# Kernel tuning notes

Measured on AMD Instinct MI355X. Metric: run time of the kernel, lower is better.

Reference implementation:

```python
import jax, jax.numpy as jnp
import numpy as np

B, T, NH, HD, VD = 2, 2048, 16, 128, 256
KD = NH * HD            # 2048
VDIM = NH * VD          # 4096
EPS = 1e-12


def _l2norm(x):
    # torch.nn.functional.normalize: x / max(||x||_2, eps)
    n = jnp.sqrt(jnp.sum(x * x, axis=-1, keepdims=True))
    return x / jnp.maximum(n, EPS)


def setup_inputs() -> dict:
    key = jax.random.key(0)
    k1, k2 = jax.random.split(key)
    x = jax.random.normal(k1, (B, T, KD), dtype=jnp.float32)
    W = jax.random.normal(k2, (2 * KD + VDIM + 2 * NH, KD), dtype=jnp.float32) * 0.02
    state = jnp.zeros((B, NH, VD, HD), dtype=jnp.float32)
    return {"x": x, "W": W, "state": state}


def reference(x, W, state):
    # shared projection (no bias)
    proj = jnp.einsum('btd,od->bto', x, W)  # [B,T,2*KD+VDIM+2*NH]
    q = proj[..., :KD].reshape(B, T, NH, HD)
    k = proj[..., KD:2 * KD].reshape(B, T, NH, HD)
    v = proj[..., 2 * KD:2 * KD + VDIM].reshape(B, T, NH, VD)
    g = jax.nn.sigmoid(proj[..., 2 * KD + VDIM:2 * KD + VDIM + NH])      # [B,T,NH] decay gate
    beta = jax.nn.sigmoid(proj[..., 2 * KD + VDIM + NH:])                # [B,T,NH]
    q = _l2norm(q)
    k = _l2norm(k)

    # time-major for scan
    qs = jnp.moveaxis(q, 1, 0)      # [T,B,NH,HD]
    ks = jnp.moveaxis(k, 1, 0)
    vs = jnp.moveaxis(v, 1, 0)      # [T,B,NH,VD]
    gs = jnp.moveaxis(g, 1, 0)      # [T,B,NH]
    bs = jnp.moveaxis(beta, 1, 0)

    def step(S, inp):
        # gated delta rule: S_t = g*S - g*b*(S k) k^T + b*v k^T ; o_t = S_t q
        q_t, k_t, v_t, g_t, b_t = inp
        Sk = jnp.einsum('bnvh,bnh->bnv', S, k_t)                         # [B,NH,VD]
        delta = b_t[..., None] * (v_t - g_t[..., None] * Sk)             # [B,NH,VD]
        S_new = g_t[..., None, None] * S + delta[..., None] * k_t[:, :, None, :]
        o = jnp.einsum('bnvh,bnh->bnv', S_new, q_t)                      # [B,NH,VD]
        return S_new, o

    _, out = jax.lax.scan(step, state, (qs, ks, vs, gs, bs))
    return jnp.moveaxis(out, 0, 1)  # [B,T,NH,VD]
```

## Files before the change

kernel.cpp:

```cpp
#include <hip/hip_runtime.h>
#include <hip/hip_bf16.h>
#include <cstdint>


typedef __attribute__((ext_vector_type(8))) short short8;
typedef __attribute__((ext_vector_type(4))) float f32x4;
typedef unsigned short u16;

using as1_void = __attribute__((address_space(1))) void;
using as3_void = __attribute__((address_space(3))) void;

__device__ __forceinline__ void gll16(const void* g, void* l) {
  __builtin_amdgcn_global_load_lds((const as1_void*)g, (as3_void*)l, 16, 0, 0);
}

__device__ __forceinline__ u16 bf16_rne(float f) {
  union { float f; uint32_t u; } x; x.f = f;
  uint32_t u = x.u;
  return (u16)((u + 0x7fffu + ((u >> 16) & 1u)) >> 16);
}
__device__ __forceinline__ float bf2f(u16 v) {
  union { uint32_t u; float f; } x; x.u = (uint32_t)v << 16;
  return x.f;
}

#define LGKM_BAR() do {                                      \
    asm volatile("s_waitcnt lgkmcnt(0)" ::: "memory");       \
    __builtin_amdgcn_s_barrier();                            \
    __builtin_amdgcn_sched_barrier(0);                       \
  } while (0)

#define SCHED_FENCE() __builtin_amdgcn_sched_barrier(0)
#define HW_BAR() __builtin_amdgcn_s_barrier()
#define LGKM0() asm volatile("s_waitcnt lgkmcnt(0)" ::: "memory")
#define VMCNT(n) asm volatile("s_waitcnt vmcnt(" #n ")" ::: "memory")

__global__ __launch_bounds__(256) void cvt_f32_bf16(const float* __restrict__ in,
                                                    u16* __restrict__ out, int n4) {
  int i = blockIdx.x * 256 + threadIdx.x;
  if (i < n4) {
    float4 v = ((const float4*)in)[i];
    ushort4 o;
    o.x = bf16_rne(v.x); o.y = bf16_rne(v.y);
    o.z = bf16_rne(v.z); o.w = bf16_rne(v.w);
    ((ushort4*)out)[i] = o;
  }
}

__global__ __launch_bounds__(256, 1) void gate_kernel(const float* __restrict__ x,
                                                      const float* __restrict__ W,
                                                      float* __restrict__ gbuf,
                                                      u16* __restrict__ xb) {
  const int w = threadIdx.x >> 6, lane = threadIdx.x & 63;
  const int r0 = (blockIdx.x * 4 + w) * 4;
  const float* xr = x + (size_t)r0 * 2048 + lane * 32;
  float4 xv[4][8];
#pragma unroll
  for (int i = 0; i < 4; ++i)
#pragma unroll
    for (int j = 0; j < 8; ++j)
      xv[i][j] = ((const float4*)(xr + (size_t)i * 2048))[j];
#pragma unroll
  for (int i = 0; i < 4; ++i) {
    u16* xrow = xb + (size_t)(r0 + i) * 2048 + lane * 32;
#pragma unroll
    for (int j = 0; j < 8; ++j) {
      ushort4 o;
      o.x = bf16_rne(xv[i][j].x); o.y = bf16_rne(xv[i][j].y);
      o.z = bf16_rne(xv[i][j].z); o.w = bf16_rne(xv[i][j].w);
      ((ushort4*)xrow)[j] = o;
    }
  }
  for (int col = 0; col < 32; ++col) {
    const float* wp = W + (size_t)(8192 + col) * 2048 + lane * 32;
    float4 wv[8];
#pragma unroll
    for (int j = 0; j < 8; ++j) wv[j] = ((const float4*)wp)[j];
    float d[4] = {0.f, 0.f, 0.f, 0.f};
#pragma unroll
    for (int i = 0; i < 4; ++i)
#pragma unroll
      for (int j = 0; j < 8; ++j)
        d[i] += xv[i][j].x * wv[j].x + xv[i][j].y * wv[j].y +
                xv[i][j].z * wv[j].z + xv[i][j].w * wv[j].w;
#pragma unroll
    for (int i = 0; i < 4; ++i) {
      d[i] += __shfl_xor(d[i], 1);  d[i] += __shfl_xor(d[i], 2);
      d[i] += __shfl_xor(d[i], 4);  d[i] += __shfl_xor(d[i], 8);
      d[i] += __shfl_xor(d[i], 16); d[i] += __shfl_xor(d[i], 32);
    }
    if (lane == 0) {
#pragma unroll
      for (int i = 0; i < 4; ++i) {
        int rv = r0 + i, b = rv >> 11, t = rv & 2047;
        float s = 1.f / (1.f + __expf(-d[i]));
        gbuf[((size_t)(b * 16 + (col & 15)) * 2048 + t) * 2 + (col >> 4)] = s;
      }
    }
  }
}

__global__ __launch_bounds__(512, 2) void gemm_bf16_btn(const u16* __restrict__ A,
                                                        const u16* __restrict__ B,
                                                        u16* __restrict__ qb,
                                                        u16* __restrict__ kb,
                                                        u16* __restrict__ vb) {
  __shared__ __align__(16) u16 As[2][16384];
  __shared__ __align__(16) u16 Bs[2][16384];
  __shared__ float nrm[2][4][128];

  const int tid = threadIdx.x;
  const int wid = tid >> 6, lane = tid & 63;
  const int lr = lane & 15, lk = lane >> 4;
  const int wr = wid >> 2, wc = wid & 3;

  const int wg = ((blockIdx.x & 7) << 6) | (blockIdx.x >> 3);
  const int bm = wg >> 5, bn = wg & 31;

  const int e8s = (tid & 7) ^ (((tid >> 3) & 1) << 2) ^ (((tid >> 5) & 1) << 1);
  const int srow = tid >> 3;
  const u16* Agb = A + (size_t)(bm * 256 + srow) * 2048 + e8s * 8;
  const u16* Bgb = B + (size_t)(bn * 256 + srow) * 2048 + e8s * 8;

  const int kkx = lr & 1;
  const int lkp = lk ^ (((lr >> 2) & 1) << 1);
  const int aOff0 = (wr * 128 + lr) * 64 + kkx * 32 + lkp * 8;
  const int aOff1 = (wr * 128 + lr) * 64 + (1 ^ kkx) * 32 + lkp * 8;
  const int bOff0 = (wc * 64 + lr) * 64 + kkx * 32 + lkp * 8;
  const int bOff1 = (wc * 64 + lr) * 64 + (1 ^ kkx) * 32 + lkp * 8;

  auto stageA = [&](int bf, int kt, int h) {
    const u16* s = Agb + (size_t)(h * 128) * 2048 + kt * 64;
    u16* d = &As[bf][h * 8192 + wid * 512];
    gll16(s, d);
    gll16(s + (size_t)64 * 2048, d + 4096);
  };
  auto stageB = [&](int bf, int kt, int h) {
    const u16* s = Bgb + (size_t)(h * 128) * 2048 + kt * 64;
    u16* d = &Bs[bf][h * 8192 + wid * 512];
    gll16(s, d);
    gll16(s + (size_t)64 * 2048, d + 4096);
  };

  f32x4 acc[8][4] = {};

  stageA(0, 0, 0); stageA(0, 0, 1);
  stageB(0, 0, 0); stageB(0, 0, 1);
  stageA(1, 1, 0); stageA(1, 1, 1);
  stageB(1, 1, 0);
  VMCNT(6);
  SCHED_FENCE();
  HW_BAR();

#define QUAD(M0, N0)                                                          \
  do {                                                                        \
    __builtin_amdgcn_s_setprio(1);                                            \
    _Pragma("unroll")                                                         \
    for (int m_ = 0; m_ < 4; ++m_)                                            \
      _Pragma("unroll")                                                       \
      for (int n_ = 0; n_ < 2; ++n_) {                                        \
        acc[M0 + m_][N0 + n_] = __builtin_amdgcn_mfma_f32_16x16x32_bf16(      \
            a[M0 + m_][0], b[N0 + n_][0], acc[M0 + m_][N0 + n_], 0, 0, 0);    \
        acc[M0 + m_][N0 + n_] = __builtin_amdgcn_mfma_f32_16x16x32_bf16(      \
            a[M0 + m_][1], b[N0 + n_][1], acc[M0 + m_][N0 + n_], 0, 0, 0);    \
      }                                                                       \
    __builtin_amdgcn_s_setprio(0);                                            \
  } while (0)

  for (int kt = 0; kt < 32; ++kt) {
    const int bf = kt & 1;
    const u16* pA0 = &As[bf][aOff0];
    const u16* pA1 = &As[bf][aOff1];
    const u16* pB0 = &Bs[bf][bOff0];
    const u16* pB1 = &Bs[bf][bOff1];
    short8 a[8][2], b[4][2];

#pragma unroll
    for (int m = 0; m < 8; ++m) {
      a[m][0] = *(const short8*)(pA0 + m * 1024);
      a[m][1] = *(const short8*)(pA1 + m * 1024);
    }
#pragma unroll
    for (int n = 0; n < 2; ++n) {
      b[n][0] = *(const short8*)(pB0 + n * 1024);
      b[n][1] = *(const short8*)(pB1 + n * 1024);
    }
    SCHED_FENCE();
    if (kt < 31) stageB((kt + 1) & 1, kt + 1, 1);
    SCHED_FENCE(); HW_BAR(); LGKM0(); SCHED_FENCE();
    QUAD(0, 0);
    SCHED_FENCE(); HW_BAR();

#pragma unroll
    for (int n = 2; n < 4; ++n) {
      b[n][0] = *(const short8*)(pB0 + n * 1024);
      b[n][1] = *(const short8*)(pB1 + n * 1024);
    }
    SCHED_FENCE();
    if (kt < 30) stageA(bf, kt + 2, 0);
    SCHED_FENCE(); HW_BAR(); LGKM0(); SCHED_FENCE();
    QUAD(0, 2);
    SCHED_FENCE(); HW_BAR();

    if (kt < 30) stageA(bf, kt + 2, 1);
    SCHED_FENCE(); HW_BAR(); SCHED_FENCE();
    QUAD(4, 0);
    SCHED_FENCE(); HW_BAR();

    if (kt < 30) stageB(bf, kt + 2, 0);
    SCHED_FENCE(); HW_BAR(); SCHED_FENCE();
    QUAD(4, 2);
    SCHED_FENCE();
    if (kt < 30) { VMCNT(6); } else if (kt == 30) { VMCNT(0); }
    SCHED_FENCE(); HW_BAR();
  }
#undef QUAD

  if (bn < 16) {
#pragma unroll
    for (int m = 0; m < 8; ++m)
#pragma unroll
      for (int r = 0; r < 4; ++r) {
        float s = 0.f;
#pragma unroll
        for (int nn = 0; nn < 4; ++nn) {
          float v = bf2f(bf16_rne(acc[m][nn][r]));
          s += v * v;
        }
        s += __shfl_xor(s, 1); s += __shfl_xor(s, 2);
        s += __shfl_xor(s, 4); s += __shfl_xor(s, 8);
        if (lr == 0) nrm[wr][wc][m * 16 + lk * 4 + r] = s;
      }
    __syncthreads();
#pragma unroll
    for (int m = 0; m < 8; ++m)
#pragma unroll
      for (int r = 0; r < 4; ++r) {
        int rloc = m * 16 + lk * 4 + r;
        float ss = nrm[wr][wc][rloc] + nrm[wr][wc ^ 1][rloc];
        float sc = 1.f / fmaxf(sqrtf(ss), 1e-12f);
        int row = bm * 256 + wr * 128 + rloc;
        int bb = row >> 11, tt = row & 2047;
#pragma unroll
        for (int nn = 0; nn < 4; ++nn) {
          int col = bn * 256 + wc * 64 + nn * 16 + lr;
          int head = (col >> 7) & 15;
          int h = col & 127;
          u16 val = bf16_rne(bf2f(bf16_rne(acc[m][nn][r])) * sc);
          u16* dst = (col < 2048) ? qb : kb;
          dst[((size_t)(bb * 16 + head) * 2048 + tt) * 128 + h] = val;
        }
      }
  } else {
#pragma unroll
    for (int m = 0; m < 8; ++m)
#pragma unroll
      for (int nn = 0; nn < 4; ++nn)
#pragma unroll
        for (int r = 0; r < 4; ++r) {
          int row = bm * 256 + wr * 128 + m * 16 + lk * 4 + r;
          int col = bn * 256 + wc * 64 + nn * 16 + lr;
          int bb = row >> 11, tt = row & 2047;
          u16 val = bf16_rne(acc[m][nn][r]);
          int vh = col - 4096;
          vb[((size_t)(bb * 16 + (vh >> 8)) * 2048 + tt) * 256 + (vh & 255)] = val;
        }
  }
}

__global__ __launch_bounds__(256) void chunk_prep(const u16* __restrict__ qb,
                                                  const u16* __restrict__ kb,
                                                  const float* __restrict__ gbuf,
                                                  float* __restrict__ gp,
                                                  u16* __restrict__ Tm,
                                                  u16* __restrict__ Pm) {
  __shared__ u16 Kc[64 * 128];
  __shared__ u16 Qc[64 * 128];
  __shared__ u16 Nn[64 * 64];
  __shared__ u16 NT[64 * 64];
  __shared__ u16 Tt[64 * 64];
  __shared__ u16 TTt[64 * 64];
  __shared__ float gl[256];
  __shared__ float Lw[64];
  __shared__ float bw[64];

  const int bid = blockIdx.x;
  const int seq = bid >> 5, c = bid & 31;
  const int t0 = c * 64;
  const int tid = threadIdx.x;
  const int w = tid >> 6, lane = tid & 63;
  const int lr = lane & 15, lk = lane >> 4;
  const int lr7 = lr & 7;

  {
    const int rowo = lane >> 4;
    const int c8e = (lane & 15) ^ rowo;
    const int c8o = (lane & 15) ^ (4 | rowo);
    if (w == 0) {
      const u16* se = kb + ((size_t)seq * 2048 + t0 + rowo) * 128 + c8e * 8;
      const u16* so = kb + ((size_t)seq * 2048 + t0 + rowo) * 128 + c8o * 8;
#pragma unroll
      for (int i = 0; i < 16; ++i)
        gll16(((i & 1) ? so : se) + (size_t)i * 512, &Kc[i * 512]);
    } else if (w == 1) {
      const u16* se = qb + ((size_t)seq * 2048 + t0 + rowo) * 128 + c8e * 8;
      const u16* so = qb + ((size_t)seq * 2048 + t0 + rowo) * 128 + c8o * 8;
#pragma unroll
      for (int i = 0; i < 16; ++i)
        gll16(((i & 1) ? so : se) + (size_t)i * 512, &Qc[i * 512]);
    } else if (w == 2) {
      gll16(gbuf + (size_t)seq * 4096 + c * 128 + lane * 4, &gl[0]);
    }
  }
  __syncthreads();

  if (w == 0) {
    float g = gl[2 * lane], b = gl[2 * lane + 1];
    float lg = __logf(g);
#pragma unroll
    for (int d = 1; d < 64; d <<= 1) {
      float y = __shfl_up(lg, d);
      if (lane >= d) lg += y;
    }
    Lw[lane] = lg;
    bw[lane] = b;
    float G = __expf(lg);
    float L63 = __shfl(lg, 63);
    float wgt = __expf(L63 - lg);
    float* gpo = gp + ((size_t)seq * 32 + c) * 256;
    gpo[lane] = b;
    gpo[64 + lane] = b * G;
    gpo[128 + lane] = G;
    gpo[192 + lane] = wgt;
  }
  __syncthreads();

  f32x4 kkacc[4] = {}, qkacc[4] = {};
#pragma unroll
  for (int ct = 0; ct < 4; ++ct)
#pragma unroll
    for (int k0 = 0; k0 < 4; ++k0) {
      const int sl = ((k0 * 4 + lk) ^ lr7) << 3;
      short8 bfr = *(const short8*)&Kc[(ct * 16 + lr) * 128 + sl];
      short8 afk = *(const short8*)&Kc[(w * 16 + lr) * 128 + sl];
      short8 afq = *(const short8*)&Qc[(w * 16 + lr) * 128 + sl];
      kkacc[ct] = __builtin_amdgcn_mfma_f32_16x16x32_bf16(afk, bfr, kkacc[ct], 0, 0, 0);
      qkacc[ct] = __builtin_amdgcn_mfma_f32_16x16x32_bf16(afq, bfr, qkacc[ct], 0, 0, 0);
    }
  u16* Pout = Pm + ((size_t)seq * 32 + c) * 4096;
#pragma unroll
  for (int ct = 0; ct < 4; ++ct)
#pragma unroll
    for (int r = 0; r < 4; ++r) {
      int s = w * 16 + lk * 4 + r;
      int cc = ct * 16 + lr;
      int iA = s * 64 + ((((ct * 2 + (lr >> 3)) ^ (s & 7)) << 3)) + lr7;
      int iB = cc * 64 + ((((s >> 3) ^ lr7) << 3)) + (s & 7);
      u16 nv = 0;
      if (cc < s)
        nv = bf16_rne(-(bw[s] * __expf(Lw[s] - Lw[cc]) * kkacc[ct][r]));
      Nn[iA] = nv;
      NT[iB] = nv;
      u16 tv = (cc == s) ? (u16)0x3F80 : nv;
      Tt[iA] = tv;
      TTt[iB] = tv;
      u16 pv = 0;
      if (cc <= s)
        pv = bf16_rne(__expf(Lw[s] - Lw[cc]) * qkacc[ct][r]);
      Pout[s * 64 + cc] = pv;
    }
  __syncthreads();

  u16* Tout = Tm + ((size_t)seq * 32 + c) * 4096;
#pragma unroll 1
  for (int j = 0; j < 5; ++j) {
    f32x4 acc2[4] = {};
#pragma unroll
    for (int ct = 0; ct < 4; ++ct)
#pragma unroll
      for (int k0 = 0; k0 < 2; ++k0) {
        const int sl = ((k0 * 4 + lk) ^ lr7) << 3;
        short8 af = *(const short8*)&Nn[(w * 16 + lr) * 64 + sl];
        short8 bfr = *(const short8*)&NT[(ct * 16 + lr) * 64 + sl];
        acc2[ct] = __builtin_amdgcn_mfma_f32_16x16x32_bf16(af, bfr, acc2[ct], 0, 0, 0);
      }
    __syncthreads();
#pragma unroll
    for (int ct = 0; ct < 4; ++ct)
#pragma unroll
      for (int r = 0; r < 4; ++r) {
        int s = w * 16 + lk * 4 + r, cc = ct * 16 + lr;
        int iA = s * 64 + ((((ct * 2 + (lr >> 3)) ^ (s & 7)) << 3)) + lr7;
        int iB = cc * 64 + ((((s >> 3) ^ lr7) << 3)) + (s & 7);
        u16 v = bf16_rne(acc2[ct][r]);
        Nn[iA] = v;
        NT[iB] = v;
      }
    __syncthreads();
    f32x4 acc3[4];
#pragma unroll
    for (int ct = 0; ct < 4; ++ct)
#pragma unroll
      for (int r = 0; r < 4; ++r) {
        int a = w * 16 + lk * 4 + r;
        acc3[ct][r] = bf2f(Tt[a * 64 + ((((ct * 2 + (lr >> 3)) ^ (a & 7)) << 3)) + lr7]);
      }
#pragma unroll
    for (int ct = 0; ct < 4; ++ct)
#pragma unroll
      for (int k0 = 0; k0 < 2; ++k0) {
        const int sl = ((k0 * 4 + lk) ^ lr7) << 3;
        short8 af = *(const short8*)&Nn[(w * 16 + lr) * 64 + sl];
        short8 bfr = *(const short8*)&TTt[(ct * 16 + lr) * 64 + sl];
        acc3[ct] = __builtin_amdgcn_mfma_f32_16x16x32_bf16(af, bfr, acc3[ct], 0, 0, 0);
      }
    __syncthreads();
    if (j < 4) {
#pragma unroll
      for (int ct = 0; ct < 4; ++ct)
#pragma unroll
        for (int r = 0; r < 4; ++r) {
          int s = w * 16 + lk * 4 + r, cc = ct * 16 + lr;
          int iA = s * 64 + ((((ct * 2 + (lr >> 3)) ^ (s & 7)) << 3)) + lr7;
          int iB = cc * 64 + ((((s >> 3) ^ lr7) << 3)) + (s & 7);
          u16 v = bf16_rne(acc3[ct][r]);
          Tt[iA] = v;
          TTt[iB] = v;
        }
      __syncthreads();
    } else {
#pragma unroll
      for (int ct = 0; ct < 4; ++ct)
#pragma unroll
        for (int r = 0; r < 4; ++r) {
          int s = w * 16 + lk * 4 + r, cc = ct * 16 + lr;
          Tout[s * 64 + cc] = bf16_rne(acc3[ct][r]);
        }
    }
  }
}

__global__ __launch_bounds__(512) void chunk_scan(const u16* __restrict__ qb,
                                                  const u16* __restrict__ kb,
                                                  const u16* __restrict__ vb,
                                                  const float* __restrict__ gp,
                                                  const u16* __restrict__ Tm,
                                                  const u16* __restrict__ Pm,
                                                  const float* __restrict__ st0,
                                                  float* __restrict__ out) {
  __shared__ u16 Kc[2][64 * 128];
  __shared__ u16 Qc[2][64 * 128];
  __shared__ u16 Vc[2][64 * 32];
  __shared__ u16 Tc[2][64 * 64];
  __shared__ u16 Pc[2][64 * 64];
  __shared__ float gpl[2][256];
  __shared__ u16 KTw[128 * 64];
  __shared__ u16 Sb[32 * 128];
  __shared__ u16 RT[32 * 64];
  __shared__ u16 UT[32 * 64];

  const int bid = blockIdx.x;
  const int shard = bid >> 5, seq = bid & 31;
  const int vs0 = shard * 32;
  const int b = seq >> 4, n = seq & 15;
  const int tid = threadIdx.x;
  const int w = tid >> 6, lane = tid & 63;
  const int lr = lane & 15, lk = lane >> 4;
  const int lr7 = lr & 7;
  const int w3 = w & 3;
  const int vt = w & 1, hgb = (w >> 1) * 2;

  const u16* kbase = kb + (size_t)seq * 2048 * 128;
  const u16* qbase = qb + (size_t)seq * 2048 * 128;
  const u16* vbase = vb + (size_t)seq * 2048 * 256 + vs0;
  const float* gpbase = gp + (size_t)seq * 32 * 256;
  const u16* Tbase = Tm + (size_t)seq * 32 * 4096;
  const u16* Pbase = Pm + (size_t)seq * 32 * 4096;

  const int rowo = lane >> 4;
  const int c8e = (lane & 15) ^ rowo;
  const int c8o = (lane & 15) ^ (4 | rowo);
  const int tp8 = (lane & 7) ^ (lane >> 3);
  const int vc8 = (lane & 3) ^ (lane >> 4);

  auto stage = [&](int sb, int c) {
    const int t0 = c * 64;
    if (w == 0 || w == 4) {
      const int i0 = (w == 0) ? 0 : 8;
      const u16* se = kbase + (size_t)(t0 + rowo) * 128 + c8e * 8;
      const u16* so = kbase + (size_t)(t0 + rowo) * 128 + c8o * 8;
#pragma unroll
      for (int i = 0; i < 8; ++i) {
        const int ii = i0 + i;
        gll16(((ii & 1) ? so : se) + (size_t)ii * 512, &Kc[sb][ii * 512]);
      }
    } else if (w == 1 || w == 5) {
      const int i0 = (w == 1) ? 0 : 8;
      const u16* se = qbase + (size_t)(t0 + rowo) * 128 + c8e * 8;
      const u16* so = qbase + (size_t)(t0 + rowo) * 128 + c8o * 8;
#pragma unroll
      for (int i = 0; i < 8; ++i) {
        const int ii = i0 + i;
        gll16(((ii & 1) ? so : se) + (size_t)ii * 512, &Qc[sb][ii * 512]);
      }
    } else if (w == 2) {
      const u16* srcT = Tbase + (size_t)c * 4096 + (lane >> 3) * 64 + tp8 * 8;
#pragma unroll
      for (int i = 0; i < 8; ++i) gll16(srcT + (size_t)i * 512, &Tc[sb][i * 512]);
    } else if (w == 6) {
      const u16* srcP = Pbase + (size_t)c * 4096 + (lane >> 3) * 64 + tp8 * 8;
#pragma unroll
      for (int i = 0; i < 8; ++i) gll16(srcP + (size_t)i * 512, &Pc[sb][i * 512]);
    } else if (w == 3) {
      const u16* src = vbase + (size_t)(t0 + (lane >> 2)) * 256 + vc8 * 8;
#pragma unroll
      for (int i = 0; i < 4; ++i) gll16(src + (size_t)i * 4096, &Vc[sb][i * 512]);
    } else {
      gll16(gpbase + (size_t)c * 256 + lane * 4, &gpl[sb][0]);
    }
  };

  f32x4 s_acc[2];
  {
    const float* s0p = st0 + ((size_t)seq * 256 + vs0) * 128;
#pragma unroll
    for (int ht = 0; ht < 2; ++ht)
#pragma unroll
      for (int r = 0; r < 4; ++r)
        s_acc[ht][r] = s0p[(size_t)(vt * 16 + lk * 4 + r) * 128 + (hgb + ht) * 16 + lr];
  }
  stage(0, 0);
  __syncthreads();

  for (int c = 0; c < 32; ++c) {
    const int buf = c & 1;
    const int t0 = c * 64;

    stage(buf ^ 1, (c < 31) ? c + 1 : 31);
#pragma unroll
    for (int ht = 0; ht < 2; ++ht)
#pragma unroll
      for (int r = 0; r < 4; ++r) {
        int row = vt * 16 + lk * 4 + r;
        int c8 = (hgb + ht) * 2 + (lr >> 3);
        Sb[row * 128 + ((c8 ^ (row & 7)) << 3) + lr7] = bf16_rne(s_acc[ht][r]);
      }
    LGKM_BAR();

    f32x4 mm_acc[2] = {};
    if (w < 4) {
#pragma unroll
      for (int ct = 0; ct < 2; ++ct)
#pragma unroll
        for (int k0 = 0; k0 < 4; ++k0) {
          const int sl = ((k0 * 4 + lk) ^ lr7) << 3;
          short8 bfr = *(const short8*)&Sb[(ct * 16 + lr) * 128 + sl];
          short8 afk = *(const short8*)&Kc[buf][(w3 * 16 + lr) * 128 + sl];
          mm_acc[ct] = __builtin_amdgcn_mfma_f32_16x16x32_bf16(afk, bfr, mm_acc[ct], 0, 0, 0);
        }
#pragma unroll
      for (int ct = 0; ct < 2; ++ct)
#pragma unroll
        for (int r = 0; r < 4; ++r) {
          int t = w3 * 16 + lk * 4 + r;
          int j2 = ct * 16 + lr;
          float bt = gpl[buf][t], bG = gpl[buf][64 + t];
          float vv = bf2f(Vc[buf][t * 32 + ((((ct * 2 + (lr >> 3)) ^ lk)) << 3) + lr7]);
          float rv = bt * vv - bG * mm_acc[ct][r];
          RT[j2 * 64 + (((t >> 3) ^ lr7) << 3) + (t & 7)] = bf16_rne(rv);
        }
    } else {
#pragma unroll
      for (int ct = 0; ct < 2; ++ct)
#pragma unroll
        for (int k0 = 0; k0 < 4; ++k0) {
          const int sl = ((k0 * 4 + lk) ^ lr7) << 3;
          short8 bfr = *(const short8*)&Sb[(ct * 16 + lr) * 128 + sl];
          short8 afq = *(const short8*)&Qc[buf][(w3 * 16 + lr) * 128 + sl];
          mm_acc[ct] = __builtin_amdgcn_mfma_f32_16x16x32_bf16(afq, bfr, mm_acc[ct], 0, 0, 0);
        }
    }
    LGKM_BAR();

    if (w < 4) {
      f32x4 u_acc[2] = {};
#pragma unroll
      for (int ct = 0; ct < 2; ++ct)
#pragma unroll
        for (int k0 = 0; k0 < 2; ++k0) {
          const int sl = ((k0 * 4 + lk) ^ lr7) << 3;
          short8 af = *(const short8*)&Tc[buf][(w3 * 16 + lr) * 64 + sl];
          short8 bfr = *(const short8*)&RT[(ct * 16 + lr) * 64 + sl];
          u_acc[ct] = __builtin_amdgcn_mfma_f32_16x16x32_bf16(af, bfr, u_acc[ct], 0, 0, 0);
        }
#pragma unroll
      for (int ct = 0; ct < 2; ++ct)
#pragma unroll
        for (int r = 0; r < 4; ++r) {
          int s2 = w3 * 16 + lk * 4 + r;
          int j2 = ct * 16 + lr;
          UT[j2 * 64 + (((s2 >> 3) ^ lr7) << 3) + (s2 & 7)] = bf16_rne(u_acc[ct][r]);
        }
    } else {
      const int s = (tid - 256) >> 2;
      const int cb0 = (tid & 3) * 4;
      const float ws = gpl[buf][192 + s];
#pragma unroll
      for (int q = 0; q < 4; ++q) {
        const int cb = cb0 + q;
        short8 kv = *(const short8*)&Kc[buf][s * 128 + ((cb ^ (s & 7)) << 3)];
#pragma unroll
        for (int j = 0; j < 8; ++j) {
          int row = cb * 8 + j;
          KTw[row * 64 + (((s >> 3) ^ (j & 7)) << 3) + (s & 7)] =
              bf16_rne(ws * bf2f((u16)kv[j]));
        }
      }
    }
    LGKM_BAR();

    {
      const float Gc = gpl[buf][128 + 63];
#pragma unroll
      for (int ht = 0; ht < 2; ++ht) {
        s_acc[ht][0] *= Gc; s_acc[ht][1] *= Gc;
        s_acc[ht][2] *= Gc; s_acc[ht][3] *= Gc;
      }
#pragma unroll
      for (int ht = 0; ht < 2; ++ht)
#pragma unroll
        for (int k0 = 0; k0 < 2; ++k0) {
          const int sl = ((k0 * 4 + lk) ^ lr7) << 3;
          short8 af = *(const short8*)&UT[(vt * 16 + lr) * 64 + sl];
          short8 bfr = *(const short8*)&KTw[((hgb + ht) * 16 + lr) * 64 + sl];
          s_acc[ht] = __builtin_amdgcn_mfma_f32_16x16x32_bf16(af, bfr, s_acc[ht], 0, 0, 0);
        }
    }
    if (w >= 4) {
      f32x4 o_acc[2];
#pragma unroll
      for (int ct = 0; ct < 2; ++ct)
#pragma unroll
        for (int r = 0; r < 4; ++r) {
          int t = w3 * 16 + lk * 4 + r;
          o_acc[ct][r] = gpl[buf][128 + t] * mm_acc[ct][r];
        }
#pragma unroll
      for (int ct = 0; ct < 2; ++ct)
#pragma unroll
        for (int k0 = 0; k0 < 2; ++k0) {
          const int sl = ((k0 * 4 + lk) ^ lr7) << 3;
          short8 af = *(const short8*)&Pc[buf][(w3 * 16 + lr) * 64 + sl];
          short8 bfr = *(const short8*)&UT[(ct * 16 + lr) * 64 + sl];
          o_acc[ct] = __builtin_amdgcn_mfma_f32_16x16x32_bf16(af, bfr, o_acc[ct], 0, 0, 0);
        }
#pragma unroll
      for (int ct = 0; ct < 2; ++ct)
#pragma unroll
        for (int r = 0; r < 4; ++r) {
          int t = w3 * 16 + lk * 4 + r;
          int j2 = ct * 16 + lr;
          out[(((size_t)b * 2048 + t0 + t) * 16 + n) * 256 + vs0 + j2] = o_acc[ct][r];
        }
    }
    __syncthreads();
  }
}

extern "C" void kernel_launch(void* const* d_in, const int* in_sizes, int n_in,
                              void* d_out, int out_size, void* d_ws, size_t ws_size,
                              hipStream_t stream) {
  const float* x = (const float*)d_in[0];
  const float* W = (const float*)d_in[1];
  const float* st0 = (const float*)d_in[2];
  float* out = (float*)d_out;
  char* ws = (char*)d_ws;

  u16* xb   = (u16*)ws;
  u16* Wb   = (u16*)(ws + 16777216);
  u16* qb   = (u16*)(ws + 50331648);
  u16* kb   = (u16*)(ws + 67108864);
  u16* vb   = (u16*)(ws + 83886080);
  float* gb = (float*)(ws + 117440512);
  float* gp = (float*)(ws + 123731968);
  u16* Tm   = (u16*)(ws + 125829120);
  u16* Pm   = (u16*)(ws + 134217728);

  cvt_f32_bf16<<<16384, 256, 0, stream>>>(W, Wb, 4194304);
  gate_kernel<<<256, 256, 0, stream>>>(x, W, gb, xb);
  gemm_bf16_btn<<<512, 512, 0, stream>>>(xb, Wb, qb, kb, vb);
  chunk_prep<<<1024, 256, 0, stream>>>(qb, kb, gb, gp, Tm, Pm);
  chunk_scan<<<256, 512, 0, stream>>>(qb, kb, vb, gp, Tm, Pm, st0, out);
}
```

Measured before the change: 350.2 us.

## Restructure GEMM LDS layout to fragment-major and reorder B staging pipeline

Changes the projection GEMM's LDS tile layout so each wave's 16-row MFMA fragment is stored contiguously (lane*8 addressing) instead of the swizzled row layout. A and B fragments are now read with simple strided offsets. The block-to-tile mapping is changed to group tiles by XCD. The B-half-0 prefetch for the next k-tile moves earlier, with the quad order changed to match and the vmcnt thresholds adjusted. It aims to reduce LDS bank conflicts and address arithmetic and to improve L2 locality per XCD, but changes the global load pattern to 16 rows × 128 B per wave and the pipeline depth for B.

```diff
diff --git a/kernel.cpp b/kernel.cpp
--- a/kernel.cpp
+++ b/kernel.cpp
@@ -114,41 +114,35 @@
   const int lr = lane & 15, lk = lane >> 4;
   const int wr = wid >> 2, wc = wid & 3;
 
-  const int wg = ((blockIdx.x & 7) << 6) | (blockIdx.x >> 3);
-  const int bm = wg >> 5, bn = wg & 31;
-
-  const int e8s = (tid & 7) ^ (((tid >> 3) & 1) << 2) ^ (((tid >> 5) & 1) << 1);
-  const int srow = tid >> 3;
-  const u16* Agb = A + (size_t)(bm * 256 + srow) * 2048 + e8s * 8;
-  const u16* Bgb = B + (size_t)(bn * 256 + srow) * 2048 + e8s * 8;
-
-  const int kkx = lr & 1;
-  const int lkp = lk ^ (((lr >> 2) & 1) << 1);
-  const int aOff0 = (wr * 128 + lr) * 64 + kkx * 32 + lkp * 8;
-  const int aOff1 = (wr * 128 + lr) * 64 + (1 ^ kkx) * 32 + lkp * 8;
-  const int bOff0 = (wc * 64 + lr) * 64 + kkx * 32 + lkp * 8;
-  const int bOff1 = (wc * 64 + lr) * 64 + (1 ^ kkx) * 32 + lkp * 8;
+  const int xcd = blockIdx.x & 7, jb = blockIdx.x >> 3;
+  const int bm = (xcd >> 2) * 8 + (jb & 7);
+  const int bn = (xcd & 3) * 8 + (jb >> 3);
+
+  const u16* Asrc = A + (size_t)(bm * 256 + wid * 16 + lr) * 2048 + lk * 8;
+  const u16* Bsrc = B + (size_t)(bn * 256 + (wid >> 2) * 64 + (wid & 3) * 16 + lr) * 2048 + lk * 8;
 
   auto stageA = [&](int bf, int kt, int h) {
-    const u16* s = Agb + (size_t)(h * 128) * 2048 + kt * 64;
-    u16* d = &As[bf][h * 8192 + wid * 512];
+    const u16* s = Asrc + (size_t)(h * 128) * 2048 + kt * 64;
+    u16* d = &As[bf][(h * 16 + wid * 2) * 512];
     gll16(s, d);
-    gll16(s + (size_t)64 * 2048, d + 4096);
+    gll16(s + 32, d + 512);
   };
   auto stageB = [&](int bf, int kt, int h) {
-    const u16* s = Bgb + (size_t)(h * 128) * 2048 + kt * 64;
-    u16* d = &Bs[bf][h * 8192 + wid * 512];
+    const u16* s = Bsrc + (size_t)(h * 128) * 2048 + kt * 64;
+    u16* d = &Bs[bf][(h * 16 + wid * 2) * 512];
     gll16(s, d);
-    gll16(s + (size_t)64 * 2048, d + 4096);
+    gll16(s + 32, d + 512);
   };
+
+  const int aBase = wr * 8192 + lane * 8;
+  const int bBase = wc * 4096 + lane * 8;
 
   f32x4 acc[8][4] = {};
 
   stageA(0, 0, 0); stageA(0, 0, 1);
   stageB(0, 0, 0); stageB(0, 0, 1);
   stageA(1, 1, 0); stageA(1, 1, 1);
-  stageB(1, 1, 0);
-  VMCNT(6);
+  VMCNT(4);
   SCHED_FENCE();
   HW_BAR();
 
@@ -169,32 +163,41 @@
 
   for (int kt = 0; kt < 32; ++kt) {
     const int bf = kt & 1;
-    const u16* pA0 = &As[bf][aOff0];
-    const u16* pA1 = &As[bf][aOff1];
-    const u16* pB0 = &Bs[bf][bOff0];
-    const u16* pB1 = &Bs[bf][bOff1];
+    const u16* pA = &As[bf][aBase];
+    const u16* pB = &Bs[bf][bBase];
     short8 a[8][2], b[4][2];
 
 #pragma unroll
-    for (int m = 0; m < 8; ++m) {
-      a[m][0] = *(const short8*)(pA0 + m * 1024);
-      a[m][1] = *(const short8*)(pA1 + m * 1024);
+    for (int m = 0; m < 4; ++m) {
+      a[m][0] = *(const short8*)(pA + (m * 2 + 0) * 512);
+      a[m][1] = *(const short8*)(pA + (m * 2 + 1) * 512);
     }
 #pragma unroll
     for (int n = 0; n < 2; ++n) {
-      b[n][0] = *(const short8*)(pB0 + n * 1024);
-      b[n][1] = *(const short8*)(pB1 + n * 1024);
+      b[n][0] = *(const short8*)(pB + (n * 2 + 0) * 512);
+      b[n][1] = *(const short8*)(pB + (n * 2 + 1) * 512);
     }
     SCHED_FENCE();
-    if (kt < 31) stageB((kt + 1) & 1, kt + 1, 1);
+    if (kt < 31) stageB(bf ^ 1, kt + 1, 1);
     SCHED_FENCE(); HW_BAR(); LGKM0(); SCHED_FENCE();
     QUAD(0, 0);
     SCHED_FENCE(); HW_BAR();
 
 #pragma unroll
+    for (int m = 4; m < 8; ++m) {
+      a[m][0] = *(const short8*)(pA + (m * 2 + 0) * 512);
+      a[m][1] = *(const short8*)(pA + (m * 2 + 1) * 512);
+    }
+    SCHED_FENCE();
+    if (kt < 31) stageB(bf ^ 1, kt + 1, 0);
+    SCHED_FENCE(); HW_BAR(); LGKM0(); SCHED_FENCE();
+    QUAD(4, 0);
+    SCHED_FENCE(); HW_BAR();
+
+#pragma unroll
     for (int n = 2; n < 4; ++n) {
-      b[n][0] = *(const short8*)(pB0 + n * 1024);
-      b[n][1] = *(const short8*)(pB1 + n * 1024);
+      b[n][0] = *(const short8*)(pB + (n * 2 + 0) * 512);
+      b[n][1] = *(const short8*)(pB + (n * 2 + 1) * 512);
     }
     SCHED_FENCE();
     if (kt < 30) stageA(bf, kt + 2, 0);
@@ -204,14 +207,9 @@
 
     if (kt < 30) stageA(bf, kt + 2, 1);
     SCHED_FENCE(); HW_BAR(); SCHED_FENCE();
-    QUAD(4, 0);
-    SCHED_FENCE(); HW_BAR();
-
-    if (kt < 30) stageB(bf, kt + 2, 0);
-    SCHED_FENCE(); HW_BAR(); SCHED_FENCE();
     QUAD(4, 2);
     SCHED_FENCE();
-    if (kt < 30) { VMCNT(6); } else if (kt == 30) { VMCNT(0); }
+    if (kt < 30) { VMCNT(4); } else if (kt == 30) { VMCNT(0); }
     SCHED_FENCE(); HW_BAR();
   }
 #undef QUAD
```

Result: slower. 370.8 us (+5.9%).
